# Kernel optimization log

Measured on AMD Instinct MI355X. Metric: run time of the kernel, lower is better.

The kernel has to match this reference:

```python
import jax, jax.numpy as jnp
import numpy as np

MODEL_DIM = 2048
RANK = 128
N_HEADS = 16
B, S = 4, 2048


def setup_inputs() -> dict:
    key = jax.random.key(0)
    k_x, k_q, k_k, k_v, k_o = jax.random.split(key, 5)
    X = jax.random.normal(k_x, (B, S, MODEL_DIM), dtype=jnp.float32)
    mask = jnp.ones((B, S, S), dtype=bool)
    W_Q = jax.random.normal(k_q, (MODEL_DIM, RANK * N_HEADS), dtype=jnp.float32)
    W_K = jax.random.normal(k_k, (MODEL_DIM, RANK * N_HEADS), dtype=jnp.float32)
    W_V = jax.random.normal(k_v, (MODEL_DIM, RANK * N_HEADS), dtype=jnp.float32)
    W_O = jax.random.normal(k_o, (RANK * N_HEADS, RANK), dtype=jnp.float32)
    return {"X": X, "mask": mask, "W_Q": W_Q, "W_K": W_K, "W_V": W_V, "W_O": W_O}


def reference(X, mask, W_Q, W_K, W_V, W_O):
    b, s, _ = X.shape
    scale = 1.0 / (RANK ** 0.5)
    # project and split heads: (b, s, h*r) -> (b, h, s, r)
    def split_heads(Y):
        return Y.reshape(b, s, N_HEADS, RANK).transpose(0, 2, 1, 3)
    Q = split_heads(X @ W_Q)
    K = split_heads(X @ W_K)
    V = split_heads(X @ W_V)
    scores = jnp.einsum('bhir,bhjr->bhij', Q, K) * scale
    scores = jnp.where(mask[:, None, :, :], scores, -jnp.inf)
    probs = jax.nn.softmax(scores, axis=-1)
    attn = jnp.einsum('bhij,bhjr->bhir', probs, V)
    attn = attn.transpose(0, 2, 1, 3).reshape(b, s, N_HEADS * RANK)
    return attn @ W_O
```

## Files before the change

### kernel.cpp

```cpp
#include <hip/hip_runtime.h>
#include <cstdint>
#include <math.h>

typedef short bf16x8 __attribute__((ext_vector_type(8)));
typedef float f32x4 __attribute__((ext_vector_type(4)));

__device__ __forceinline__ unsigned short f2bf(float x) {
  union { float f; uint32_t u; } v; v.f = x;
  return (unsigned short)((v.u + 0x7FFFu + ((v.u >> 16) & 1u)) >> 16);
}
__device__ __forceinline__ float bf2f(unsigned short h) {
  union { uint32_t u; float f; } v; v.u = ((uint32_t)h) << 16;
  return v.f;
}

__device__ __forceinline__ void ld_lds16(const unsigned short* g, unsigned short* l) {
  auto gp = (const __attribute__((address_space(1))) unsigned short*)(uintptr_t)g;
  auto lp = (__attribute__((address_space(3))) unsigned short*)(uint32_t)(uintptr_t)l;
  __builtin_amdgcn_global_load_lds(gp, lp, 16, 0, 0);
}

#define DMA_COL(lane) ((((lane) & 3) ^ (((lane) >> 3) & 3)) * 8)
#define SWZ(l15) ((((l15) >> 1) & 3) * 8)
#define DMA_COL64(lane) ((((lane) & 7) ^ (((lane) >> 3) & 7)) * 8)

__global__ __launch_bounds__(256) void split_f32(const float* __restrict__ src,
                                                 unsigned short* __restrict__ hi,
                                                 unsigned short* __restrict__ lo, int n) {
  int i = (blockIdx.x * 256 + threadIdx.x) * 4;
  if (i >= n) return;
  float4 v = *(const float4*)(src + i);
  ushort4 h, l;
  h.x = f2bf(v.x); l.x = f2bf(v.x - bf2f(h.x));
  h.y = f2bf(v.y); l.y = f2bf(v.y - bf2f(h.y));
  h.z = f2bf(v.z); l.z = f2bf(v.z - bf2f(h.z));
  h.w = f2bf(v.w); l.w = f2bf(v.w - bf2f(h.w));
  *(ushort4*)(hi + i) = h;
  *(ushort4*)(lo + i) = l;
}

template<bool LO>
__global__ __launch_bounds__(256) void tsplit(const float* __restrict__ W,
                                              unsigned short* __restrict__ hiT,
                                              unsigned short* __restrict__ loT,
                                              int K, int N) {
  __shared__ float tile[32][33];
  const int tx = threadIdx.x, ty = threadIdx.y;
  const int bx = blockIdx.x, by = blockIdx.y;
#pragma unroll
  for (int i = 0; i < 4; ++i)
    tile[ty + i * 8][tx] = W[(size_t)(by * 32 + ty + i * 8) * N + bx * 32 + tx];
  __syncthreads();
#pragma unroll
  for (int i = 0; i < 4; ++i) {
    float v = tile[tx][ty + i * 8];
    size_t o = (size_t)(bx * 32 + ty + i * 8) * K + by * 32 + tx;
    unsigned short h = f2bf(v);
    hiT[o] = h;
    if (LO) loT[o] = f2bf(v - bf2f(h));
  }
}

__global__ __launch_bounds__(512, 2) void gemm_qkv2(
    const unsigned short* __restrict__ Xhi, const unsigned short* __restrict__ Xlo,
    const unsigned short* __restrict__ Wq_h, const unsigned short* __restrict__ Wq_l,
    const unsigned short* __restrict__ Wk_h, const unsigned short* __restrict__ Wk_l,
    const unsigned short* __restrict__ Wv_h,
    unsigned short* __restrict__ Qhi, unsigned short* __restrict__ Qlo,
    unsigned short* __restrict__ Khi, unsigned short* __restrict__ Klo,
    unsigned short* __restrict__ Vt, float qscale) {
  __shared__ unsigned short sm[3 * 24576];
  const int K = 2048, N = 2048;
  const int z = blockIdx.z;
  const int t = threadIdx.x;
  const int wave = t >> 6, lane = t & 63, quad = lane >> 4, l15 = lane & 15;
  const int m0 = blockIdx.y * 256, n0 = blockIdx.x * 128;
  const int wm = (wave >> 1) * 64, wn = (wave & 1) * 64;
  f32x4 acc[4][4] = {};

  if (z < 2) {
    const unsigned short* Bhi = z ? Wk_h : Wq_h;
    const unsigned short* Blo = z ? Wk_l : Wq_l;
    const int cq0 = (quad * 8) ^ SWZ(l15);
    const unsigned short* gch[6];
    int loff[6];
#pragma unroll
    for (int j = 0; j < 6; ++j) {
      const int c = wave * 6 + j;
      const unsigned short* base; int row0, toff, rg;
      if (c < 16)      { base = Xhi; row0 = m0; toff = 0;     rg = c; }
      else if (c < 32) { base = Xlo; row0 = m0; toff = 8192;  rg = c - 16; }
      else if (c < 40) { base = Bhi; row0 = n0; toff = 16384; rg = c - 32; }
      else             { base = Blo; row0 = n0; toff = 20480; rg = c - 40; }
      gch[j] = base + (size_t)(row0 + rg * 16 + (lane >> 2)) * K + DMA_COL(lane);
      loff[j] = toff + rg * 512;
    }
    auto stage = [&](int buf, int k0) {
#pragma unroll
      for (int j = 0; j < 6; ++j)
        ld_lds16(gch[j] + k0, sm + buf * 24576 + loff[j]);
    };
    stage(0, 0);
    stage(1, 32);
    asm volatile("s_waitcnt vmcnt(6)" ::: "memory");
    __builtin_amdgcn_s_barrier();
    __builtin_amdgcn_sched_barrier(0);
    int cur = 0, st = 2;
    for (int tix = 0; tix < 64; ++tix) {
      if (tix + 2 < 64) stage(st, (tix + 2) * 32);
      const unsigned short* bufp = sm + cur * 24576;
      bf16x8 ah[4], al[4], bh[4], bl[4];
#pragma unroll
      for (int mb = 0; mb < 4; ++mb) {
        ah[mb] = *(const bf16x8*)&bufp[(wm + mb * 16 + l15) * 32 + cq0];
        al[mb] = *(const bf16x8*)&bufp[8192 + (wm + mb * 16 + l15) * 32 + cq0];
      }
#pragma unroll
      for (int nb = 0; nb < 4; ++nb) {
        bh[nb] = *(const bf16x8*)&bufp[16384 + (wn + nb * 16 + l15) * 32 + cq0];
        bl[nb] = *(const bf16x8*)&bufp[20480 + (wn + nb * 16 + l15) * 32 + cq0];
      }
      __builtin_amdgcn_s_setprio(1);
#pragma unroll
      for (int mb = 0; mb < 4; ++mb)
#pragma unroll
        for (int nb = 0; nb < 4; ++nb) {
          acc[mb][nb] = __builtin_amdgcn_mfma_f32_16x16x32_bf16(ah[mb], bh[nb], acc[mb][nb], 0, 0, 0);
          acc[mb][nb] = __builtin_amdgcn_mfma_f32_16x16x32_bf16(ah[mb], bl[nb], acc[mb][nb], 0, 0, 0);
          acc[mb][nb] = __builtin_amdgcn_mfma_f32_16x16x32_bf16(al[mb], bh[nb], acc[mb][nb], 0, 0, 0);
        }
      __builtin_amdgcn_s_setprio(0);
      if (tix + 2 < 64) asm volatile("s_waitcnt vmcnt(6)" ::: "memory");
      else              asm volatile("s_waitcnt vmcnt(0)" ::: "memory");
      __builtin_amdgcn_s_barrier();
      __builtin_amdgcn_sched_barrier(0);
      cur = cur == 2 ? 0 : cur + 1;
      st = st == 2 ? 0 : st + 1;
    }
    const float osc = z ? 1.0f : qscale;
    unsigned short* oh = z ? Khi : Qhi;
    unsigned short* ol = z ? Klo : Qlo;
#pragma unroll
    for (int mb = 0; mb < 4; ++mb)
#pragma unroll
      for (int nb = 0; nb < 4; ++nb)
#pragma unroll
        for (int r = 0; r < 4; ++r) {
          int row = m0 + wm + mb * 16 + quad * 4 + r;
          int col = n0 + wn + nb * 16 + l15;
          float v = acc[mb][nb][r] * osc;
          unsigned short h = f2bf(v);
          oh[(size_t)row * N + col] = h;
          ol[(size_t)row * N + col] = f2bf(v - bf2f(h));
        }
  } else {
    const unsigned short* gch[6];
    int loff[6];
#pragma unroll
    for (int j = 0; j < 6; ++j) {
      const int c = wave * 6 + j;
      const unsigned short* base; int row0, toff, rg;
      if (c < 32) { base = Xhi;  row0 = m0; toff = 0;     rg = c; }
      else        { base = Wv_h; row0 = n0; toff = 16384; rg = c - 32; }
      gch[j] = base + (size_t)(row0 + rg * 8 + (lane >> 3)) * K + DMA_COL64(lane);
      loff[j] = toff + rg * 512;
    }
    auto stage = [&](int buf, int k0) {
#pragma unroll
      for (int j = 0; j < 6; ++j)
        ld_lds16(gch[j] + k0, sm + buf * 24576 + loff[j]);
    };
    stage(0, 0);
    stage(1, 64);
    asm volatile("s_waitcnt vmcnt(6)" ::: "memory");
    __builtin_amdgcn_s_barrier();
    __builtin_amdgcn_sched_barrier(0);
    int cur = 0, st = 2;
    for (int tix = 0; tix < 32; ++tix) {
      if (tix + 2 < 32) stage(st, (tix + 2) * 64);
      const unsigned short* bufp = sm + cur * 24576;
      bf16x8 a[2][4], b[2][4];
#pragma unroll
      for (int kk = 0; kk < 2; ++kk) {
#pragma unroll
        for (int mb = 0; mb < 4; ++mb) {
          const int row = wm + mb * 16 + l15;
          a[kk][mb] = *(const bf16x8*)&bufp[row * 64 + (((kk * 4 + quad) ^ (row & 7)) * 8)];
        }
#pragma unroll
        for (int nb = 0; nb < 4; ++nb) {
          const int row = wn + nb * 16 + l15;
          b[kk][nb] = *(const bf16x8*)&bufp[16384 + row * 64 + (((kk * 4 + quad) ^ (row & 7)) * 8)];
        }
      }
      __builtin_amdgcn_s_setprio(1);
#pragma unroll
      for (int kk = 0; kk < 2; ++kk)
#pragma unroll
        for (int mb = 0; mb < 4; ++mb)
#pragma unroll
          for (int nb = 0; nb < 4; ++nb)
            acc[mb][nb] = __builtin_amdgcn_mfma_f32_16x16x32_bf16(a[kk][mb], b[kk][nb], acc[mb][nb], 0, 0, 0);
      __builtin_amdgcn_s_setprio(0);
      if (tix + 2 < 32) asm volatile("s_waitcnt vmcnt(6)" ::: "memory");
      else              asm volatile("s_waitcnt vmcnt(0)" ::: "memory");
      __builtin_amdgcn_s_barrier();
      __builtin_amdgcn_sched_barrier(0);
      cur = cur == 2 ? 0 : cur + 1;
      st = st == 2 ? 0 : st + 1;
    }
#pragma unroll
    for (int mb = 0; mb < 4; ++mb)
#pragma unroll
      for (int nb = 0; nb < 4; ++nb) {
        ushort4 pk;
        pk.x = f2bf(acc[mb][nb][0]);
        pk.y = f2bf(acc[mb][nb][1]);
        pk.z = f2bf(acc[mb][nb][2]);
        pk.w = f2bf(acc[mb][nb][3]);
        *(ushort4*)&sm[(wn + nb * 16 + l15) * 264 + wm + mb * 16 + quad * 4] = pk;
      }
    __syncthreads();
    const int bb = m0 >> 11;
    const int mloc = m0 & 2047;
    unsigned short* Vb = Vt + (size_t)bb * 2048 * 2048;
#pragma unroll
    for (int jj = 0; jj < 8; ++jj) {
      int idx = jj * 512 + t;
      int n = idx >> 5, mu = idx & 31;
      uint4 v = *(uint4*)&sm[n * 264 + mu * 8];
      *(uint4*)(Vb + (size_t)(n0 + n) * 2048 + mloc + mu * 8) = v;
    }
  }
}

__global__ __launch_bounds__(256) void gemm_out(
    const unsigned short* __restrict__ Ahi, const unsigned short* __restrict__ Bhi,
    float* __restrict__ out, int M, int N, int K, int ldk) {
  __shared__ unsigned short sm[8192];
  unsigned short* Ah = sm;
  unsigned short* Bh = sm + 4096;
  const int z = blockIdx.z;
  const int t = threadIdx.x;
  const int wave = t >> 6, lane = t & 63, quad = lane >> 4, l15 = lane & 15;
  const int wm = (wave & 1) * 64, wn = (wave >> 1) * 64;
  const int m0 = blockIdx.y * 128, n0 = blockIdx.x * 128;
  const int cq0 = (quad * 8) ^ SWZ(l15);
  const unsigned short* gsrc = (wave < 2) ? Ahi : Bhi;
  unsigned short* ldst = (wave < 2) ? Ah : Bh;
  const int row0 = (wave < 2) ? m0 : n0;
  const int jb = (wave & 1) * 4;
  const unsigned short* gbase = gsrc + (size_t)(row0 + (lane >> 2)) * K + DMA_COL(lane);
  f32x4 acc[4][4] = {};
  for (int k0 = z * ldk; k0 < (z + 1) * ldk; k0 += 32) {
#pragma unroll
    for (int j = 0; j < 4; ++j)
      ld_lds16(gbase + (size_t)((jb + j) * 16) * K + k0, ldst + (jb + j) * 512);
    __syncthreads();
    bf16x8 ah[4], bh[4];
#pragma unroll
    for (int mb = 0; mb < 4; ++mb)
      ah[mb] = *(bf16x8*)&Ah[(wm + mb * 16 + l15) * 32 + cq0];
#pragma unroll
    for (int nb = 0; nb < 4; ++nb)
      bh[nb] = *(bf16x8*)&Bh[(wn + nb * 16 + l15) * 32 + cq0];
#pragma unroll
    for (int mb = 0; mb < 4; ++mb)
#pragma unroll
      for (int nb = 0; nb < 4; ++nb)
        acc[mb][nb] = __builtin_amdgcn_mfma_f32_16x16x32_bf16(ah[mb], bh[nb], acc[mb][nb], 0, 0, 0);
    __syncthreads();
  }
  float* of = out + (size_t)z * M * N;
#pragma unroll
  for (int mb = 0; mb < 4; ++mb)
#pragma unroll
    for (int nb = 0; nb < 4; ++nb)
#pragma unroll
      for (int r = 0; r < 4; ++r) {
        int row = m0 + wm + mb * 16 + quad * 4 + r;
        int col = n0 + wn + nb * 16 + l15;
        of[(size_t)row * N + col] = acc[mb][nb][r];
      }
}

__global__ __launch_bounds__(256) void reduceN(const float* __restrict__ p,
                                               float* __restrict__ out, int n, int nsl) {
  int i = (blockIdx.x * 256 + threadIdx.x) * 4;
  if (i >= n) return;
  float4 acc = *(const float4*)(p + i);
  for (int s = 1; s < nsl; ++s) {
    float4 v = *(const float4*)(p + (size_t)s * n + i);
    acc.x += v.x; acc.y += v.y; acc.z += v.z; acc.w += v.w;
  }
  *(float4*)(out + i) = acc;
}

__global__ __launch_bounds__(256, 2) void attn_mfma(
    const unsigned short* __restrict__ Qhi, const unsigned short* __restrict__ Qlo,
    const unsigned short* __restrict__ Khi, const unsigned short* __restrict__ Klo,
    const unsigned short* __restrict__ Vt, unsigned short* __restrict__ Ob, int S) {
  __shared__ unsigned short Kh_s[3 * 4096];
  __shared__ unsigned short Kl_s[3 * 4096];
  __shared__ unsigned short V_s[3 * 4096];
  __shared__ unsigned short P_s[4 * 640];
  const int t = threadIdx.x;
  const int wave = t >> 6, lane = t & 63, quad = lane >> 4, l15 = lane & 15;
  const int bidall = blockIdx.x;
  const size_t boff = (size_t)(bidall >> 9) * (2048 * 2048);
  Qhi += boff; Qlo += boff; Khi += boff; Klo += boff; Vt += boff; Ob += boff;
  const int bid = bidall & 511;
  const int xcd = bid & 7, slot = bid >> 3;
  const int head = (xcd << 1) | (slot >> 5);
  const int qblk = slot & 31;
  const int q_base = qblk * 64 + wave * 16;
  const size_t hoff = (size_t)head * 128;
  const int cq0 = (quad * 8) ^ SWZ(l15);

  bf16x8 qh[4], ql[4];
#pragma unroll
  for (int kb = 0; kb < 4; ++kb) {
    size_t off = (size_t)(q_base + l15) * 2048 + hoff + kb * 32 + quad * 8;
    qh[kb] = *(const bf16x8*)(Qhi + off);
    ql[kb] = *(const bf16x8*)(Qlo + off);
  }
  f32x4 o[8] = {};
  float m_run = -INFINITY, l_run = 0.f;

  const int lr = lane >> 2, lc = DMA_COL(lane);
  const unsigned short* gKh = Khi + (size_t)lr * 2048 + hoff + wave * 32 + lc;
  const unsigned short* gKl = Klo + (size_t)lr * 2048 + hoff + wave * 32 + lc;
  const unsigned short* gV  = Vt + (hoff + wave * 32 + lr) * (size_t)S + lc;
  unsigned short* Pw = P_s + wave * 640;

  auto stage = [&](int buf, int kpos) {
    const int b4 = buf * 4096 + wave * 1024;
#pragma unroll
    for (int i = 0; i < 2; ++i) {
      ld_lds16(gKh + (size_t)(kpos + i * 16) * 2048, Kh_s + b4 + i * 512);
      ld_lds16(gKl + (size_t)(kpos + i * 16) * 2048, Kl_s + b4 + i * 512);
      ld_lds16(gV + (size_t)(i * 16) * S + kpos,      V_s + b4 + i * 512);
    }
  };
  stage(0, 0);
  stage(1, 32);
  asm volatile("s_waitcnt vmcnt(6)" ::: "memory");
  __builtin_amdgcn_s_barrier();
  __builtin_amdgcn_sched_barrier(0);

  int cur = 0, st = 2;
  for (int tix = 0; tix < 64; ++tix) {
    if (tix + 2 < 64) stage(st, (tix + 2) * 32);
    const int cb = cur * 4096;
    f32x4 s[2] = {};
    __builtin_amdgcn_s_setprio(1);
#pragma unroll
    for (int mb = 0; mb < 2; ++mb)
#pragma unroll
      for (int kb = 0; kb < 4; ++kb) {
        bf16x8 kh = *(bf16x8*)&Kh_s[cb + kb * 1024 + (mb * 16 + l15) * 32 + cq0];
        bf16x8 kl = *(bf16x8*)&Kl_s[cb + kb * 1024 + (mb * 16 + l15) * 32 + cq0];
        s[mb] = __builtin_amdgcn_mfma_f32_16x16x32_bf16(kh, qh[kb], s[mb], 0, 0, 0);
        s[mb] = __builtin_amdgcn_mfma_f32_16x16x32_bf16(kh, ql[kb], s[mb], 0, 0, 0);
        s[mb] = __builtin_amdgcn_mfma_f32_16x16x32_bf16(kl, qh[kb], s[mb], 0, 0, 0);
      }
    __builtin_amdgcn_s_setprio(0);
    float mt = s[0][0];
#pragma unroll
    for (int r = 1; r < 4; ++r) mt = fmaxf(mt, s[0][r]);
#pragma unroll
    for (int r = 0; r < 4; ++r) mt = fmaxf(mt, s[1][r]);
    mt = fmaxf(mt, __shfl_xor(mt, 16));
    mt = fmaxf(mt, __shfl_xor(mt, 32));
    if (!__all(mt <= m_run + 8.f)) {
      const float m_new = fmaxf(m_run, mt);
      const float alpha = __builtin_amdgcn_exp2f(m_run - m_new);
      l_run *= alpha;
#pragma unroll
      for (int rb = 0; rb < 8; ++rb)
#pragma unroll
        for (int r = 0; r < 4; ++r) o[rb][r] *= alpha;
      m_run = m_new;
    }
    float p[8];
#pragma unroll
    for (int mb = 0; mb < 2; ++mb)
#pragma unroll
      for (int r = 0; r < 4; ++r)
        p[mb * 4 + r] = __builtin_amdgcn_exp2f(s[mb][r] - m_run);
    float rs = p[0];
#pragma unroll
    for (int j = 1; j < 8; ++j) rs += p[j];
    rs += __shfl_xor(rs, 16);
    rs += __shfl_xor(rs, 32);
    l_run += rs;
#pragma unroll
    for (int mb = 0; mb < 2; ++mb) {
      ushort4 pk;
      pk.x = f2bf(p[mb * 4 + 0]);
      pk.y = f2bf(p[mb * 4 + 1]);
      pk.z = f2bf(p[mb * 4 + 2]);
      pk.w = f2bf(p[mb * 4 + 3]);
      *(ushort4*)&Pw[l15 * 40 + mb * 16 + quad * 4] = pk;
    }
    bf16x8 pf = *(bf16x8*)&Pw[l15 * 40 + quad * 8];
    __builtin_amdgcn_s_setprio(1);
#pragma unroll
    for (int rb = 0; rb < 8; ++rb) {
      bf16x8 vb = *(bf16x8*)&V_s[cb + (rb * 16 + l15) * 32 + cq0];
      o[rb] = __builtin_amdgcn_mfma_f32_16x16x32_bf16(vb, pf, o[rb], 0, 0, 0);
    }
    __builtin_amdgcn_s_setprio(0);
    if (tix + 2 < 64) asm volatile("s_waitcnt vmcnt(6)" ::: "memory");
    else              asm volatile("s_waitcnt vmcnt(0)" ::: "memory");
    __builtin_amdgcn_s_barrier();
    __builtin_amdgcn_sched_barrier(0);
    cur = cur == 2 ? 0 : cur + 1;
    st = st == 2 ? 0 : st + 1;
  }
  const float inv = 1.0f / l_run;
#pragma unroll
  for (int rb = 0; rb < 8; ++rb) {
    ushort4 pk;
    pk.x = f2bf(o[rb][0] * inv);
    pk.y = f2bf(o[rb][1] * inv);
    pk.z = f2bf(o[rb][2] * inv);
    pk.w = f2bf(o[rb][3] * inv);
    *(ushort4*)(Ob + (size_t)(q_base + l15) * 2048 + hoff + rb * 16 + quad * 4) = pk;
  }
}

extern "C" void kernel_launch(void* const* d_in, const int* in_sizes, int n_in,
                              void* d_out, int out_size, void* d_ws, size_t ws_size,
                              hipStream_t stream) {
  (void)in_sizes; (void)n_in; (void)out_size;
  const float* X   = (const float*)d_in[0];
  const float* W_Q = (const float*)d_in[2];
  const float* W_K = (const float*)d_in[3];
  const float* W_V = (const float*)d_in[4];
  const float* W_O = (const float*)d_in[5];
  float* out = (float*)d_out;

  const int S = 2048, HD = 2048;
  const size_t P = (size_t)HD * HD;
  unsigned short* w = (unsigned short*)d_ws;
  unsigned short* WqThi = w;
  unsigned short* WqTlo = w + P;
  unsigned short* WkThi = w + 2 * P;
  unsigned short* WkTlo = w + 3 * P;
  unsigned short* WvThi = w + 4 * P;
  unsigned short* WoThi = w + 5 * P;
  unsigned short* base6 = w + 5 * P + P / 16;

  const float qscale = 0.12752551286084109f;

  dim3 bT(32, 8);
  tsplit<true ><<<dim3(64, 64), bT, 0, stream>>>(W_Q, WqThi, WqTlo, HD, HD);
  tsplit<true ><<<dim3(64, 64), bT, 0, stream>>>(W_K, WkThi, WkTlo, HD, HD);
  tsplit<false><<<dim3(64, 64), bT, 0, stream>>>(W_V, WvThi, nullptr, HD, HD);
  tsplit<false><<<dim3(4, 64),  bT, 0, stream>>>(W_O, WoThi, nullptr, HD, 128);

  const size_t elW = 5 * P + P / 16;
  const size_t need2 = (elW + 14 * P) * 2;
  const size_t need1 = (elW + 7 * P) * 2;
  int C; bool tight = false;
  if (ws_size >= need2)      C = 2;
  else if (ws_size >= need1) C = 1;
  else { C = 1; tight = true; }

  const size_t CP = (size_t)C * P;
  unsigned short* Xhi = base6;
  unsigned short* Xlo = base6 + CP;
  unsigned short* Qhi = base6 + 2 * CP;
  unsigned short* Qlo = base6 + 3 * CP;
  unsigned short* Khi = base6 + 4 * CP;
  unsigned short* Klo = base6 + 5 * CP;
  unsigned short* Vt  = tight ? Xlo : base6 + 6 * CP;
  unsigned short* attnB = Xhi;
  float* fpart = (float*)Qhi;

  const int M = C * S;
  const int zn = 16 / C;
  const int ldk = HD / zn;
  const int NOUT = M * 128;

  for (int c = 0; c < 4 / C; ++c) {
    split_f32<<<C * 4096, 256, 0, stream>>>(X + (size_t)c * CP, Xhi, Xlo, (int)CP);
    gemm_qkv2<<<dim3(16, C * 8, 3), 512, 0, stream>>>(
        Xhi, Xlo, WqThi, WqTlo, WkThi, WkTlo, WvThi,
        Qhi, Qlo, Khi, Klo, Vt, qscale);
    attn_mfma<<<C * 512, 256, 0, stream>>>(Qhi, Qlo, Khi, Klo, Vt, attnB, S);
    gemm_out<<<dim3(1, C * 16, zn), 256, 0, stream>>>(attnB, WoThi, fpart, M, 128, HD, ldk);
    reduceN<<<NOUT / 1024, 256, 0, stream>>>(fpart, out + (size_t)c * NOUT, NOUT, zn);
  }
}
```

Baseline: 964.6 us.

## Process two query groups per attention wave and swizzle QKV GEMM blocks across XCDs

The attention kernel now has each wave handle two 16-row query groups (128 queries per block instead of 64). Each K/V tile staged into LDS is therefore reused for twice as many queries, and the grid is halved. The QKV GEMM also remaps its linear block id so consecutive blocks spread across the 8 XCDs, aiming for better L2 locality. The cost is about double the accumulator and Q registers per wave, which may reduce occupancy, and fewer blocks means less parallelism to hide latency.

```diff
diff --git a/kernel.cpp b/kernel.cpp
--- a/kernel.cpp
+++ b/kernel.cpp
@@ -71,10 +71,16 @@
     unsigned short* __restrict__ Vt, float qscale) {
   __shared__ unsigned short sm[3 * 24576];
   const int K = 2048, N = 2048;
-  const int z = blockIdx.z;
+  const int gx = gridDim.x, gy = gridDim.y;
+  const int T = gx * gy * gridDim.z;
+  const int lid = blockIdx.x + gx * (blockIdx.y + gy * blockIdx.z);
+  const int sl = (lid & 7) * (T >> 3) + (lid >> 3);
+  const int bx = sl % gx;
+  const int by = (sl / gx) % gy;
+  const int z  = sl / (gx * gy);
   const int t = threadIdx.x;
   const int wave = t >> 6, lane = t & 63, quad = lane >> 4, l15 = lane & 15;
-  const int m0 = blockIdx.y * 256, n0 = blockIdx.x * 128;
+  const int m0 = by * 256, n0 = bx * 128;
   const int wm = (wave >> 1) * 64, wn = (wave & 1) * 64;
   f32x4 acc[4][4] = {};
 
@@ -307,25 +313,28 @@
   const int t = threadIdx.x;
   const int wave = t >> 6, lane = t & 63, quad = lane >> 4, l15 = lane & 15;
   const int bidall = blockIdx.x;
-  const size_t boff = (size_t)(bidall >> 9) * (2048 * 2048);
+  const size_t boff = (size_t)(bidall >> 8) * (2048 * 2048);
   Qhi += boff; Qlo += boff; Khi += boff; Klo += boff; Vt += boff; Ob += boff;
-  const int bid = bidall & 511;
+  const int bid = bidall & 255;
   const int xcd = bid & 7, slot = bid >> 3;
-  const int head = (xcd << 1) | (slot >> 5);
-  const int qblk = slot & 31;
-  const int q_base = qblk * 64 + wave * 16;
+  const int head = (xcd << 1) | (slot >> 4);
+  const int qblk = slot & 15;
   const size_t hoff = (size_t)head * 128;
   const int cq0 = (quad * 8) ^ SWZ(l15);
 
-  bf16x8 qh[4], ql[4];
-#pragma unroll
-  for (int kb = 0; kb < 4; ++kb) {
-    size_t off = (size_t)(q_base + l15) * 2048 + hoff + kb * 32 + quad * 8;
-    qh[kb] = *(const bf16x8*)(Qhi + off);
-    ql[kb] = *(const bf16x8*)(Qlo + off);
-  }
-  f32x4 o[8] = {};
-  float m_run = -INFINITY, l_run = 0.f;
+  bf16x8 qh[2][4], ql[2][4];
+#pragma unroll
+  for (int g = 0; g < 2; ++g) {
+    const int qb = qblk * 128 + g * 64 + wave * 16;
+#pragma unroll
+    for (int kb = 0; kb < 4; ++kb) {
+      size_t off = (size_t)(qb + l15) * 2048 + hoff + kb * 32 + quad * 8;
+      qh[g][kb] = *(const bf16x8*)(Qhi + off);
+      ql[g][kb] = *(const bf16x8*)(Qlo + off);
+    }
+  }
+  f32x4 o[2][8] = {};
+  float m_run[2] = {-INFINITY, -INFINITY}, l_run[2] = {0.f, 0.f};
 
   const int lr = lane >> 2, lc = DMA_COL(lane);
   const unsigned short* gKh = Khi + (size_t)lr * 2048 + hoff + wave * 32 + lc;
@@ -352,7 +361,7 @@
   for (int tix = 0; tix < 64; ++tix) {
     if (tix + 2 < 64) stage(st, (tix + 2) * 32);
     const int cb = cur * 4096;
-    f32x4 s[2] = {};
+    f32x4 s[2][2] = {};
     __builtin_amdgcn_s_setprio(1);
 #pragma unroll
     for (int mb = 0; mb < 2; ++mb)
@@ -360,55 +369,64 @@
       for (int kb = 0; kb < 4; ++kb) {
         bf16x8 kh = *(bf16x8*)&Kh_s[cb + kb * 1024 + (mb * 16 + l15) * 32 + cq0];
         bf16x8 kl = *(bf16x8*)&Kl_s[cb + kb * 1024 + (mb * 16 + l15) * 32 + cq0];
-        s[mb] = __builtin_amdgcn_mfma_f32_16x16x32_bf16(kh, qh[kb], s[mb], 0, 0, 0);
-        s[mb] = __builtin_amdgcn_mfma_f32_16x16x32_bf16(kh, ql[kb], s[mb], 0, 0, 0);
-        s[mb] = __builtin_amdgcn_mfma_f32_16x16x32_bf16(kl, qh[kb], s[mb], 0, 0, 0);
+        s[0][mb] = __builtin_amdgcn_mfma_f32_16x16x32_bf16(kh, qh[0][kb], s[0][mb], 0, 0, 0);
+        s[0][mb] = __builtin_amdgcn_mfma_f32_16x16x32_bf16(kh, ql[0][kb], s[0][mb], 0, 0, 0);
+        s[0][mb] = __builtin_amdgcn_mfma_f32_16x16x32_bf16(kl, qh[0][kb], s[0][mb], 0, 0, 0);
+        s[1][mb] = __builtin_amdgcn_mfma_f32_16x16x32_bf16(kh, qh[1][kb], s[1][mb], 0, 0, 0);
+        s[1][mb] = __builtin_amdgcn_mfma_f32_16x16x32_bf16(kh, ql[1][kb], s[1][mb], 0, 0, 0);
+        s[1][mb] = __builtin_amdgcn_mfma_f32_16x16x32_bf16(kl, qh[1][kb], s[1][mb], 0, 0, 0);
       }
     __builtin_amdgcn_s_setprio(0);
-    float mt = s[0][0];
-#pragma unroll
-    for (int r = 1; r < 4; ++r) mt = fmaxf(mt, s[0][r]);
-#pragma unroll
-    for (int r = 0; r < 4; ++r) mt = fmaxf(mt, s[1][r]);
-    mt = fmaxf(mt, __shfl_xor(mt, 16));
-    mt = fmaxf(mt, __shfl_xor(mt, 32));
-    if (!__all(mt <= m_run + 8.f)) {
-      const float m_new = fmaxf(m_run, mt);
-      const float alpha = __builtin_amdgcn_exp2f(m_run - m_new);
-      l_run *= alpha;
-#pragma unroll
-      for (int rb = 0; rb < 8; ++rb)
-#pragma unroll
-        for (int r = 0; r < 4; ++r) o[rb][r] *= alpha;
-      m_run = m_new;
-    }
-    float p[8];
-#pragma unroll
-    for (int mb = 0; mb < 2; ++mb)
-#pragma unroll
-      for (int r = 0; r < 4; ++r)
-        p[mb * 4 + r] = __builtin_amdgcn_exp2f(s[mb][r] - m_run);
-    float rs = p[0];
-#pragma unroll
-    for (int j = 1; j < 8; ++j) rs += p[j];
-    rs += __shfl_xor(rs, 16);
-    rs += __shfl_xor(rs, 32);
-    l_run += rs;
-#pragma unroll
-    for (int mb = 0; mb < 2; ++mb) {
-      ushort4 pk;
-      pk.x = f2bf(p[mb * 4 + 0]);
-      pk.y = f2bf(p[mb * 4 + 1]);
-      pk.z = f2bf(p[mb * 4 + 2]);
-      pk.w = f2bf(p[mb * 4 + 3]);
-      *(ushort4*)&Pw[l15 * 40 + mb * 16 + quad * 4] = pk;
-    }
-    bf16x8 pf = *(bf16x8*)&Pw[l15 * 40 + quad * 8];
+
+    bf16x8 pf[2];
+#pragma unroll
+    for (int g = 0; g < 2; ++g) {
+      float mt = s[g][0][0];
+#pragma unroll
+      for (int r = 1; r < 4; ++r) mt = fmaxf(mt, s[g][0][r]);
+#pragma unroll
+      for (int r = 0; r < 4; ++r) mt = fmaxf(mt, s[g][1][r]);
+      mt = fmaxf(mt, __shfl_xor(mt, 16));
+      mt = fmaxf(mt, __shfl_xor(mt, 32));
+      if (!__all(mt <= m_run[g] + 8.f)) {
+        const float m_new = fmaxf(m_run[g], mt);
+        const float alpha = __builtin_amdgcn_exp2f(m_run[g] - m_new);
+        l_run[g] *= alpha;
+#pragma unroll
+        for (int rb = 0; rb < 8; ++rb)
+#pragma unroll
+          for (int r = 0; r < 4; ++r) o[g][rb][r] *= alpha;
+        m_run[g] = m_new;
+      }
+      float p[8];
+#pragma unroll
+      for (int mb = 0; mb < 2; ++mb)
+#pragma unroll
+        for (int r = 0; r < 4; ++r)
+          p[mb * 4 + r] = __builtin_amdgcn_exp2f(s[g][mb][r] - m_run[g]);
+      float rs = p[0];
+#pragma unroll
+      for (int j = 1; j < 8; ++j) rs += p[j];
+      rs += __shfl_xor(rs, 16);
+      rs += __shfl_xor(rs, 32);
+      l_run[g] += rs;
+#pragma unroll
+      for (int mb = 0; mb < 2; ++mb) {
+        ushort4 pk;
+        pk.x = f2bf(p[mb * 4 + 0]);
+        pk.y = f2bf(p[mb * 4 + 1]);
+        pk.z = f2bf(p[mb * 4 + 2]);
+        pk.w = f2bf(p[mb * 4 + 3]);
+        *(ushort4*)&Pw[l15 * 40 + mb * 16 + quad * 4] = pk;
+      }
+      pf[g] = *(bf16x8*)&Pw[l15 * 40 + quad * 8];
+    }
     __builtin_amdgcn_s_setprio(1);
 #pragma unroll
     for (int rb = 0; rb < 8; ++rb) {
       bf16x8 vb = *(bf16x8*)&V_s[cb + (rb * 16 + l15) * 32 + cq0];
-      o[rb] = __builtin_amdgcn_mfma_f32_16x16x32_bf16(vb, pf, o[rb], 0, 0, 0);
+      o[0][rb] = __builtin_amdgcn_mfma_f32_16x16x32_bf16(vb, pf[0], o[0][rb], 0, 0, 0);
+      o[1][rb] = __builtin_amdgcn_mfma_f32_16x16x32_bf16(vb, pf[1], o[1][rb], 0, 0, 0);
     }
     __builtin_amdgcn_s_setprio(0);
     if (tix + 2 < 64) asm volatile("s_waitcnt vmcnt(6)" ::: "memory");
@@ -418,15 +436,19 @@
     cur = cur == 2 ? 0 : cur + 1;
     st = st == 2 ? 0 : st + 1;
   }
-  const float inv = 1.0f / l_run;
-#pragma unroll
-  for (int rb = 0; rb < 8; ++rb) {
-    ushort4 pk;
-    pk.x = f2bf(o[rb][0] * inv);
-    pk.y = f2bf(o[rb][1] * inv);
-    pk.z = f2bf(o[rb][2] * inv);
-    pk.w = f2bf(o[rb][3] * inv);
-    *(ushort4*)(Ob + (size_t)(q_base + l15) * 2048 + hoff + rb * 16 + quad * 4) = pk;
+#pragma unroll
+  for (int g = 0; g < 2; ++g) {
+    const int qb = qblk * 128 + g * 64 + wave * 16;
+    const float inv = 1.0f / l_run[g];
+#pragma unroll
+    for (int rb = 0; rb < 8; ++rb) {
+      ushort4 pk;
+      pk.x = f2bf(o[g][rb][0] * inv);
+      pk.y = f2bf(o[g][rb][1] * inv);
+      pk.z = f2bf(o[g][rb][2] * inv);
+      pk.w = f2bf(o[g][rb][3] * inv);
+      *(ushort4*)(Ob + (size_t)(qb + l15) * 2048 + hoff + rb * 16 + quad * 4) = pk;
+    }
   }
 }
 
@@ -489,7 +511,7 @@
     gemm_qkv2<<<dim3(16, C * 8, 3), 512, 0, stream>>>(
         Xhi, Xlo, WqThi, WqTlo, WkThi, WkTlo, WvThi,
         Qhi, Qlo, Khi, Klo, Vt, qscale);
-    attn_mfma<<<C * 512, 256, 0, stream>>>(Qhi, Qlo, Khi, Klo, Vt, attnB, S);
+    attn_mfma<<<C * 256, 256, 0, stream>>>(Qhi, Qlo, Khi, Klo, Vt, attnB, S);
     gemm_out<<<dim3(1, C * 16, zn), 256, 0, stream>>>(attnB, WoThi, fpart, M, 128, HD, ldk);
     reduceN<<<NOUT / 1024, 256, 0, stream>>>(fpart, out + (size_t)c * NOUT, NOUT, zn);
   }
```

After: 1.024 ms. 6.1% more time.
